# Kernel optimization log

Measured on AMD Instinct MI355X. Metric: run time of the kernel, lower is better.

The kernel has to match this reference:

```python
import jax, jax.numpy as jnp
import numpy as np

VOCAB, EMBED, HIDDEN = 32000, 256, 512
B, T = 8, 512


def setup_inputs() -> dict:
    key = jax.random.key(0)
    ks = jax.random.split(key, 7)
    x = jax.random.randint(ks[0], (B, T), 0, VOCAB)
    emb = jax.random.normal(ks[1], (VOCAB, EMBED), dtype=jnp.float32)
    W_xh = jax.random.normal(ks[2], (EMBED, HIDDEN), dtype=jnp.float32) * 0.01
    W_hh = jax.random.normal(ks[3], (HIDDEN, HIDDEN), dtype=jnp.float32) * 0.01
    b_h = jnp.zeros((HIDDEN,), dtype=jnp.float32)
    # nn.Linear(hidden*2, vocab): weight [vocab, 2*hidden], bias [vocab]
    lim = 1.0 / np.sqrt(2 * HIDDEN)
    fc_w = jax.random.uniform(ks[4], (VOCAB, 2 * HIDDEN), minval=-lim, maxval=lim, dtype=jnp.float32)
    fc_b = jax.random.uniform(ks[5], (VOCAB,), minval=-lim, maxval=lim, dtype=jnp.float32)
    return {"x": x, "emb": emb, "W_xh": W_xh, "W_hh": W_hh, "b_h": b_h, "fc_w": fc_w, "fc_b": fc_b}


def reference(x, emb, W_xh, W_hh, b_h, fc_w, fc_b):
    e = emb[x]  # [B,T,E]
    h0 = jnp.zeros((x.shape[0], W_hh.shape[0]), dtype=e.dtype)

    def step(h, xt):  # xt: [B,E]
        h = jnp.tanh(xt @ W_xh + h @ W_hh + b_h)
        return h, h

    _, H = jax.lax.scan(step, h0, jnp.swapaxes(e, 0, 1))  # H: [T,B,Hd]
    H = jnp.swapaxes(H, 0, 1)  # [B,T,Hd]
    # full (non-causal) dot-product self-attention over hidden states
    scores = jnp.einsum('bth,bsh->bts', H, H)  # [B,T,T]
    attn = jax.nn.softmax(scores, axis=-1)
    ctx = jnp.einsum('bts,bsh->bth', attn, H)  # [B,T,Hd]
    combined = jnp.concatenate([H, ctx], axis=-1)  # [B,T,2Hd]
    return combined @ fc_w.T + fc_b  # [B,T,V]
```

## Files before the change

### kernel.cpp

```cpp
#include <hip/hip_runtime.h>

typedef unsigned int u32;
typedef unsigned short u16;
typedef short bf16x8 __attribute__((ext_vector_type(8)));
typedef float f32x4 __attribute__((ext_vector_type(4)));

#define DEV __device__ __forceinline__

DEV u16 f2bf(float f) {
  u32 u = __builtin_bit_cast(u32, f);
  u += 0x7fffu + ((u >> 16) & 1u);
  return (u16)(u >> 16);
}
DEV float bf2f(u16 b) { u32 u = ((u32)b) << 16; return __builtin_bit_cast(float, u); }

DEV float dot2bf(float acc, u32 w, u32 h) {
  asm("v_dot2_f32_bf16 %0, %1, %2, %0" : "+v"(acc) : "v"(w), "v"(h));
  return acc;
}

DEV void gload16(const void* g, void* l) {
  __builtin_amdgcn_global_load_lds(
      (__attribute__((address_space(1))) void*)(void*)g,
      (__attribute__((address_space(3))) void*)l, 16, 0, 0);
}

__global__ void k_prep_fcw(const float* __restrict__ w, u16* __restrict__ o, int n4) {
  int i = blockIdx.x * blockDim.x + threadIdx.x;
  int stride = gridDim.x * blockDim.x;
  for (; i < n4; i += stride) {
    float4 v = ((const float4*)w)[i];
    ushort4 r; r.x = f2bf(v.x); r.y = f2bf(v.y); r.z = f2bf(v.z); r.w = f2bf(v.w);
    ((ushort4*)o)[i] = r;
  }
}

#define PREG 184
#define PLQ  18

__global__ void k_prep_whh(const float* __restrict__ w, u32* __restrict__ wr, u32* __restrict__ wq) {
  int idx = blockIdx.x * 256 + threadIdx.x;
  int p = idx >> 9, j = idx & 511;
  u32 word = (u32)f2bf(w[(2 * p) * 512 + j]) | ((u32)f2bf(w[(2 * p + 1) * 512 + j]) << 16);
  if (p < PREG) wr[p * 512 + j] = word;
  else { int d = p - PREG; wq[((d >> 2) * 512 + j) * 4 + (d & 3)] = word; }
}

__global__ __launch_bounds__(256) void k_embx(
    const int* __restrict__ x, const float* __restrict__ emb,
    const float* __restrict__ wxh, const float* __restrict__ bh,
    float* __restrict__ X) {
  __shared__ float sA[64][65];
  __shared__ __align__(16) float sB[64][68];
  int tid = threadIdx.x;
  int row0 = blockIdx.x * 64, col0 = blockIdx.y * 64;
  int tx = tid & 15, ty = tid >> 4;
  f32x4 acc[4] = {};
  for (int kc = 0; kc < 256; kc += 64) {
    __syncthreads();
#pragma unroll
    for (int i = 0; i < 4; ++i) {
      int f = i * 256 + tid;
      int r = f >> 4, c4 = (f & 15) * 4;
      int xr = x[row0 + r];
      float4 v = *(const float4*)&emb[(size_t)xr * 256 + kc + c4];
      sA[r][c4 + 0] = v.x; sA[r][c4 + 1] = v.y; sA[r][c4 + 2] = v.z; sA[r][c4 + 3] = v.w;
      float4 u = *(const float4*)&wxh[(size_t)(kc + r) * 512 + col0 + c4];
      *(float4*)&sB[r][c4] = u;
    }
    __syncthreads();
#pragma unroll
    for (int e = 0; e < 64; ++e) {
      f32x4 bv = *(const f32x4*)&sB[e][tx * 4];
      float a0 = sA[ty * 4 + 0][e], a1 = sA[ty * 4 + 1][e];
      float a2 = sA[ty * 4 + 2][e], a3 = sA[ty * 4 + 3][e];
      acc[0] += a0 * bv; acc[1] += a1 * bv; acc[2] += a2 * bv; acc[3] += a3 * bv;
    }
  }
  f32x4 bh4 = *(const f32x4*)&bh[col0 + tx * 4];
#pragma unroll
  for (int a = 0; a < 4; ++a) {
    f32x4 r = acc[a] + bh4;
    *(f32x4*)&X[(size_t)(row0 + ty * 4 + a) * 512 + col0 + tx * 4] = r;
  }
}

__global__ __launch_bounds__(512)
__attribute__((amdgpu_waves_per_eu(2, 2)))
void k_rnn(
    const u32* __restrict__ Wr, const u32* __restrict__ Wq,
    const float* __restrict__ X,
    u16* __restrict__ Hb16 ) {
  __shared__ __align__(16) u32 wl[PLQ * 512 * 4];
  __shared__ __align__(16) u32 hHI[2][256];
  __shared__ __align__(16) u32 hLO[2][256];
  int j = threadIdx.x;
  int b = blockIdx.x;
  u32 wreg[PREG];
#pragma unroll
  for (int p = 0; p < PREG; ++p) wreg[p] = Wr[p * 512 + j];
#pragma unroll
  for (int q = 0; q < PLQ; ++q)
    *(uint4*)&wl[(q * 512 + j) * 4] = *(const uint4*)&Wq[(q * 512 + j) * 4];
  if (j < 256) { hHI[0][j] = 0u; hLO[0][j] = 0u; }
  const float* Xb = X + (size_t)b * 512 * 512;
  u16* Hb = Hb16 + (size_t)b * 512 * 1024;
  __syncthreads();
  int cur = 0;
  float xv = Xb[j];
  for (int t = 0; t < 512; ++t) {
    int tn = t < 511 ? t + 1 : 511;
    float xnext = Xb[tn * 512 + j];
    float a0 = 0.f, a1 = 0.f, a2 = 0.f, a3 = 0.f;
    const u32* hbH = hHI[cur];
    const u32* hbL = hLO[cur];
#pragma unroll
    for (int c = 0; c < PREG / 4; ++c) {
      uint4 hH = *(const uint4*)&hbH[c * 4];
      uint4 hL = *(const uint4*)&hbL[c * 4];
      a0 = dot2bf(dot2bf(a0, wreg[c * 4 + 0], hH.x), wreg[c * 4 + 0], hL.x);
      a1 = dot2bf(dot2bf(a1, wreg[c * 4 + 1], hH.y), wreg[c * 4 + 1], hL.y);
      a2 = dot2bf(dot2bf(a2, wreg[c * 4 + 2], hH.z), wreg[c * 4 + 2], hL.z);
      a3 = dot2bf(dot2bf(a3, wreg[c * 4 + 3], hH.w), wreg[c * 4 + 3], hL.w);
    }
#pragma unroll
    for (int q = 0; q < PLQ; ++q) {
      uint4 wv = *(const uint4*)&wl[(q * 512 + j) * 4];
      uint4 hH = *(const uint4*)&hbH[PREG + q * 4];
      uint4 hL = *(const uint4*)&hbL[PREG + q * 4];
      a0 = dot2bf(dot2bf(a0, wv.x, hH.x), wv.x, hL.x);
      a1 = dot2bf(dot2bf(a1, wv.y, hH.y), wv.y, hL.y);
      a2 = dot2bf(dot2bf(a2, wv.z, hH.z), wv.z, hL.z);
      a3 = dot2bf(dot2bf(a3, wv.w, hH.w), wv.w, hL.w);
    }
    float z = xv + ((a0 + a1) + (a2 + a3));
    float ez = __expf(2.f * z);
    float h = 1.f - 2.f / (ez + 1.f);
    u16 hi = f2bf(h);
    u16 lo = f2bf(h - bf2f(hi));
    Hb[t * 1024 + j] = hi;
    ((u16*)hHI[cur ^ 1])[j] = hi;
    ((u16*)hLO[cur ^ 1])[j] = lo;
    __syncthreads();
    cur ^= 1;
    xv = xnext;
  }
}

template <int BF16OUT, int BIAS, int BF32B>
__global__ __launch_bounds__(256) void k_gemm_bt(
    const u16* __restrict__ A, int lda, long long aStr,
    const void* __restrict__ Bt_, int ldb, long long bStr,
    void* __restrict__ Cv, int ldc, long long cStr,
    int numMt, int numNt, int K, const float* __restrict__ bias) {
  __shared__ __align__(16) u16 lA[128 * 64];
  __shared__ __align__(16) u16 lB[128 * 64];
  int tid = threadIdx.x;
  int lane = tid & 63, wid = tid >> 6;
  int nwg = gridDim.x, wg = blockIdx.x;
  int q = nwg >> 3;
  int swz = (wg & 7) * q + (wg >> 3);
  int gm = numMt < 8 ? numMt : 8;
  int perg = gm * numNt;
  int grp = swz / perg;
  int rem = swz - grp * perg;
  int mt = grp * gm + rem % gm;
  int nt = rem / gm;
  int mrow = mt * 128, ncol = nt * 128;
  long long batch = blockIdx.y;
  A += batch * aStr;
  const u16* Bh = (const u16*)Bt_ + (BF32B ? 0 : batch * bStr);
  const float* Bf = (const float*)Bt_ + (BF32B ? batch * bStr : 0);
  float* Cf = (float*)Cv + batch * cStr;
  u16* Ch = (u16*)Cv + batch * cStr;

  f32x4 acc[4][4] = {};
  int wr = wid >> 1, wc = wid & 1;
  int lr = lane & 15, lk = (lane >> 4) * 8;

  for (int kt = 0; kt < K; kt += 64) {
    __syncthreads();
#pragma unroll
    for (int i = 0; i < 4; ++i) {
      int chunk = wid * 4 + i;
      int idx = chunk * 64 + lane;
      int r = idx >> 3, c = (idx & 7) * 8;
      gload16(&A[(size_t)(mrow + r) * lda + kt + c], &lA[chunk * 512]);
    }
    if constexpr (!BF32B) {
#pragma unroll
      for (int i = 0; i < 4; ++i) {
        int chunk = wid * 4 + i;
        int idx = chunk * 64 + lane;
        int r = idx >> 3, c = (idx & 7) * 8;
        gload16(&Bh[(size_t)(ncol + r) * ldb + kt + c], &lB[chunk * 512]);
      }
    } else {
#pragma unroll
      for (int u = 0; u < 8; ++u) {
        int flat = u * 1024 + tid * 4;
        int r = flat >> 6, c = flat & 63;
        float4 v = *(const float4*)&Bf[(size_t)(ncol + r) * ldb + kt + c];
        uint2 pk;
        pk.x = (u32)f2bf(v.x) | ((u32)f2bf(v.y) << 16);
        pk.y = (u32)f2bf(v.z) | ((u32)f2bf(v.w) << 16);
        *(uint2*)&lB[r * 64 + c] = pk;
      }
    }
    __syncthreads();
#pragma unroll
    for (int ks = 0; ks < 2; ++ks) {
      bf16x8 aF[4], bF[4];
#pragma unroll
      for (int mi = 0; mi < 4; ++mi)
        aF[mi] = *(const bf16x8*)&lA[(wr * 64 + mi * 16 + lr) * 64 + ks * 32 + lk];
#pragma unroll
      for (int ni = 0; ni < 4; ++ni)
        bF[ni] = *(const bf16x8*)&lB[(wc * 64 + ni * 16 + lr) * 64 + ks * 32 + lk];
#pragma unroll
      for (int mi = 0; mi < 4; ++mi)
#pragma unroll
        for (int ni = 0; ni < 4; ++ni)
          acc[mi][ni] = __builtin_amdgcn_mfma_f32_16x16x32_bf16(aF[mi], bF[ni], acc[mi][ni], 0, 0, 0);
    }
  }
  int rq = (lane >> 4) * 4;
#pragma unroll
  for (int ni = 0; ni < 4; ++ni) {
    int col = ncol + wc * 64 + ni * 16 + lr;
    float bv = BIAS ? bias[col] : 0.f;
#pragma unroll
    for (int mi = 0; mi < 4; ++mi) {
      int row = mrow + wr * 64 + mi * 16 + rq;
#pragma unroll
      for (int qq = 0; qq < 4; ++qq) {
        float v = acc[mi][ni][qq] + bv;
        if (BF16OUT) Ch[(size_t)(row + qq) * ldc + col] = f2bf(v);
        else         Cf[(size_t)(row + qq) * ldc + col] = v;
      }
    }
  }
}

DEV void stage_half(const u16* __restrict__ G, int ldg, int grow0, int kcol0,
                    u16* region, int w, int lane) {
#pragma unroll
  for (int jj = 0; jj < 2; ++jj) {
    int fb = jj * 512 + w * 64;
    int f = fb + lane;
    int r = f >> 2, s = f & 3;
    int c = (s ^ ((r >> 1) & 3)) * 8;
    gload16(&G[(size_t)(grow0 + r) * ldg + kcol0 + c], region + (size_t)fb * 8);
  }
}
DEV bf16x8 lds_frag(const u16* region, int r, int lq) {
  return *(const bf16x8*)&region[r * 32 + ((lq ^ ((r >> 1) & 3)) * 8)];
}

__global__ __launch_bounds__(512, 2) void k_gemm8(
    const u16* __restrict__ A, int lda,
    const u16* __restrict__ B, int ldb,
    float* __restrict__ C, int ldc,
    int numMt, int numNt, int K, const float* __restrict__ bias) {
  __shared__ __align__(16) u16 lds8[65536];
  int tid = threadIdx.x;
  int lane = tid & 63, wid = tid >> 6;
  int w = wid, wm = wid >> 2, wn = wid & 3;
  int lr = lane & 15, lq = lane >> 4;
  int nwg = gridDim.x, wg = blockIdx.x;
  int qd = nwg >> 3;
  int swz = (wg & 7) * qd + (wg >> 3);
  int gm = numMt < 8 ? numMt : 8;
  int perg = gm * numNt;
  int grp = swz / perg;
  int rem = swz - grp * perg;
  int mt = grp * gm + rem % gm;
  int nt = rem / gm;
  int mrow = mt * 256, ncol = nt * 256;
  int NT = K >> 6;

#define REGION(buf, op, kh) (lds8 + (((buf) * 2 + (op)) * 2 + (kh)) * 8192)

  f32x4 acc[8][4];
#pragma unroll
  for (int mi = 0; mi < 8; ++mi)
#pragma unroll
    for (int ni = 0; ni < 4; ++ni) acc[mi][ni] = (f32x4){0.f, 0.f, 0.f, 0.f};

  stage_half(A, lda, mrow, 0,  REGION(0, 0, 0), w, lane);
  stage_half(B, ldb, ncol, 0,  REGION(0, 1, 0), w, lane);
  stage_half(A, lda, mrow, 32, REGION(0, 0, 1), w, lane);
  stage_half(B, ldb, ncol, 32, REGION(0, 1, 1), w, lane);
  stage_half(A, lda, mrow, 64, REGION(1, 0, 0), w, lane);
  stage_half(B, ldb, ncol, 64, REGION(1, 1, 0), w, lane);
  asm volatile("s_waitcnt vmcnt(4)" ::: "memory");
  __builtin_amdgcn_s_barrier();
  asm volatile("" ::: "memory");

  for (int T = 0; T < NT; ++T) {
    int buf = T & 1;
    int s12 = (T + 1 < NT), s34 = (T + 2 < NT);
#pragma unroll
    for (int ph = 0; ph < 4; ++ph) {
      int ch = ph & 1, ks = ph >> 1;
      const u16* Ar = REGION(buf, 0, ks);
      const u16* Br = REGION(buf, 1, ks);
      bf16x8 aF[8], bF[2];
#pragma unroll
      for (int mi = 0; mi < 8; ++mi)
        aF[mi] = lds_frag(Ar, wm * 128 + mi * 16 + lr, lq);
#pragma unroll
      for (int nl = 0; nl < 2; ++nl)
        bF[nl] = lds_frag(Br, wn * 64 + (ch * 2 + nl) * 16 + lr, lq);
      if (ph == 0) { if (s12) stage_half(A, lda, mrow, (T + 1) * 64 + 32, REGION(buf ^ 1, 0, 1), w, lane); }
      if (ph == 1) { if (s12) stage_half(B, ldb, ncol, (T + 1) * 64 + 32, REGION(buf ^ 1, 1, 1), w, lane); }
      if (ph == 2) { if (s34) stage_half(A, lda, mrow, (T + 2) * 64,      REGION(buf, 0, 0),     w, lane); }
      if (ph == 3) { if (s34) stage_half(B, ldb, ncol, (T + 2) * 64,      REGION(buf, 1, 0),     w, lane); }
      asm volatile("" ::: "memory");
      __builtin_amdgcn_s_barrier();
      asm volatile("s_waitcnt lgkmcnt(0)" ::: "memory");
      __builtin_amdgcn_sched_barrier(0);
      __builtin_amdgcn_s_setprio(1);
#pragma unroll
      for (int mi = 0; mi < 8; ++mi) {
        acc[mi][ch * 2 + 0] = __builtin_amdgcn_mfma_f32_16x16x32_bf16(aF[mi], bF[0], acc[mi][ch * 2 + 0], 0, 0, 0);
        acc[mi][ch * 2 + 1] = __builtin_amdgcn_mfma_f32_16x16x32_bf16(aF[mi], bF[1], acc[mi][ch * 2 + 1], 0, 0, 0);
      }
      __builtin_amdgcn_s_setprio(0);
      if (ph == 3) {
        if (T >= NT - 2) asm volatile("s_waitcnt vmcnt(0)" ::: "memory");
        else             asm volatile("s_waitcnt vmcnt(4)" ::: "memory");
      }
      asm volatile("" ::: "memory");
      __builtin_amdgcn_s_barrier();
      asm volatile("" ::: "memory");
    }
  }
#undef REGION

#pragma unroll
  for (int mi = 0; mi < 8; ++mi) {
    int row0 = mrow + wm * 128 + mi * 16 + lq * 4;
#pragma unroll
    for (int ni = 0; ni < 4; ++ni) {
      int col = ncol + wn * 64 + ni * 16 + lr;
      float bv = bias[col];
#pragma unroll
      for (int rg = 0; rg < 4; ++rg)
        C[(size_t)(row0 + rg) * ldc + col] = acc[mi][ni][rg] + bv;
    }
  }
}

__global__ __launch_bounds__(256) void k_softmax(const float* __restrict__ S, u16* __restrict__ P) {
  int wid = threadIdx.x >> 6, lane = threadIdx.x & 63;
  int row = blockIdx.x * 4 + wid;
  const float* sr = S + (size_t)row * 512;
  f32x4 v0 = *(const f32x4*)&sr[lane * 4];
  f32x4 v1 = *(const f32x4*)&sr[256 + lane * 4];
  float m = fmaxf(fmaxf(fmaxf(v0.x, v0.y), fmaxf(v0.z, v0.w)),
                  fmaxf(fmaxf(v1.x, v1.y), fmaxf(v1.z, v1.w)));
#pragma unroll
  for (int o = 32; o; o >>= 1) m = fmaxf(m, __shfl_xor(m, o, 64));
  f32x4 e0, e1;
  e0.x = __expf(v0.x - m); e0.y = __expf(v0.y - m); e0.z = __expf(v0.z - m); e0.w = __expf(v0.w - m);
  e1.x = __expf(v1.x - m); e1.y = __expf(v1.y - m); e1.z = __expf(v1.z - m); e1.w = __expf(v1.w - m);
  float s = (e0.x + e0.y + e0.z + e0.w) + (e1.x + e1.y + e1.z + e1.w);
#pragma unroll
  for (int o = 32; o; o >>= 1) s += __shfl_xor(s, o, 64);
  float inv = 1.f / s;
  ushort4 o0, o1;
  o0.x = f2bf(e0.x * inv); o0.y = f2bf(e0.y * inv); o0.z = f2bf(e0.z * inv); o0.w = f2bf(e0.w * inv);
  o1.x = f2bf(e1.x * inv); o1.y = f2bf(e1.y * inv); o1.z = f2bf(e1.z * inv); o1.w = f2bf(e1.w * inv);
  *(ushort4*)&P[(size_t)row * 512 + lane * 4] = o0;
  *(ushort4*)&P[(size_t)row * 512 + 256 + lane * 4] = o1;
}

__global__ __launch_bounds__(256) void k_transpose(const u16* __restrict__ Hsrc, u16* __restrict__ HT) {
  __shared__ __align__(16) u16 tile[64][72];
  int b = blockIdx.z;
  int sb = blockIdx.x * 64, hb = blockIdx.y * 64;
  int tid = threadIdx.x;
#pragma unroll
  for (int i = 0; i < 4; ++i) {
    int f = i * 256 + tid; int r = f >> 4, c4 = (f & 15) * 4;
    ushort4 v = *(const ushort4*)&Hsrc[((size_t)(b * 512 + sb + r)) * 1024 + hb + c4];
    *(ushort4*)&tile[r][c4] = v;
  }
  __syncthreads();
#pragma unroll
  for (int i = 0; i < 4; ++i) {
    int f = i * 256 + tid; int h = f >> 4, s4 = (f & 15) * 4;
    ushort4 v;
    v.x = tile[s4 + 0][h]; v.y = tile[s4 + 1][h]; v.z = tile[s4 + 2][h]; v.w = tile[s4 + 3][h];
    *(ushort4*)&HT[((size_t)(b * 512 + hb + h)) * 512 + sb + s4] = v;
  }
}

extern "C" void kernel_launch(void* const* d_in, const int* in_sizes, int n_in,
                              void* d_out, int out_size, void* d_ws, size_t ws_size,
                              hipStream_t stream) {
  const int*   x   = (const int*)d_in[0];
  const float* emb = (const float*)d_in[1];
  const float* wxh = (const float*)d_in[2];
  const float* whh = (const float*)d_in[3];
  const float* bh  = (const float*)d_in[4];
  const float* fcw = (const float*)d_in[5];
  const float* fcb = (const float*)d_in[6];
  float* out = (float*)d_out;

  char* ws = (char*)d_ws;
  u32* Wr  = (u32*)ws;
  u32* Wq  = (u32*)(ws + 376832);
  u16* comb = (u16*)(ws + 524288);
  u16* fcwb = (u16*)(ws + 524288 + 8388608);
  bool bigws = ws_size >= (size_t)(524288 + 8388608 + 65536000);
  char* ob = (char*)d_out;
  float* X  = (float*)ob;
  float* S  = (float*)(ob + 8388608);
  u16*   P  = (u16*)(ob + 16777216);
  u16*   HT = (u16*)(ob + 20971520);

  k_prep_whh<<<dim3(512), dim3(256), 0, stream>>>(whh, Wr, Wq);
  k_embx<<<dim3(64, 8), dim3(256), 0, stream>>>(x, emb, wxh, bh, X);
  if (bigws)
    k_prep_fcw<<<dim3(2048), dim3(256), 0, stream>>>(fcw, fcwb, 8192000);
  k_rnn<<<dim3(8), dim3(512), 0, stream>>>(Wr, Wq, X, comb);
  k_gemm_bt<0, 0, 0><<<dim3(16, 8), dim3(256), 0, stream>>>(
      comb, 1024, 512LL * 1024, comb, 1024, 512LL * 1024,
      (void*)S, 512, 512LL * 512, 4, 4, 512, (const float*)nullptr);
  k_softmax<<<dim3(1024), dim3(256), 0, stream>>>(S, P);
  k_transpose<<<dim3(8, 8, 8), dim3(256), 0, stream>>>(comb, HT);
  k_gemm_bt<1, 0, 0><<<dim3(16, 8), dim3(256), 0, stream>>>(
      P, 512, 512LL * 512, HT, 512, 512LL * 512,
      (void*)(comb + 512), 1024, 512LL * 1024, 4, 4, 512, (const float*)nullptr);
  if (bigws)
    k_gemm8<<<dim3(2000), dim3(512), 0, stream>>>(
        comb, 1024, fcwb, 1024, out, 32000, 16, 125, 1024, fcb);
  else
    k_gemm_bt<0, 1, 1><<<dim3(8000), dim3(256), 0, stream>>>(
        comb, 1024, 0LL, fcw, 1024, 0LL,
        (void*)out, 32000, 0LL, 32, 250, 1024, fcb);
}
```

Baseline: 1.648 ms.

## Broadcast recurrent hidden state via readlane into SGPR operands for RNN dot products

The recurrent step now has each lane load just two uint4 chunks of an interleaved hi/lo hidden-state buffer, instead of every thread reading the whole hidden vector from LDS with uniform-address loads. Each h value is then broadcast to the wave with v_readlane and passed to v_dot2 as a scalar operand. This layout interleaves the hi and lo bf16 words so one pair of vector loads per lane covers the full 512-element state. It trades LDS traffic for many readlane instructions on the serial critical path, and hardcodes 46 register chunks, which must match PREG.

Result: slower. 2.695 ms (+63.5%).

```diff
diff --git a/kernel.cpp b/kernel.cpp
--- a/kernel.cpp
+++ b/kernel.cpp
@@ -14,8 +14,8 @@
 }
 DEV float bf2f(u16 b) { u32 u = ((u32)b) << 16; return __builtin_bit_cast(float, u); }
 
-DEV float dot2bf(float acc, u32 w, u32 h) {
-  asm("v_dot2_f32_bf16 %0, %1, %2, %0" : "+v"(acc) : "v"(w), "v"(h));
+DEV float dot2bf_s(float acc, u32 w, u32 h_uni) {
+  asm("v_dot2_f32_bf16 %0, %1, %2, %0" : "+v"(acc) : "s"(h_uni), "v"(w));
   return acc;
 }
 
@@ -92,9 +92,8 @@
     const float* __restrict__ X,
     u16* __restrict__ Hb16 ) {
   __shared__ __align__(16) u32 wl[PLQ * 512 * 4];
-  __shared__ __align__(16) u32 hHI[2][256];
-  __shared__ __align__(16) u32 hLO[2][256];
-  int j = threadIdx.x;
+  __shared__ __align__(16) u32 hch[2][512];
+  int j = threadIdx.x, lane = j & 63;
   int b = blockIdx.x;
   u32 wreg[PREG];
 #pragma unroll
@@ -102,7 +101,8 @@
 #pragma unroll
   for (int q = 0; q < PLQ; ++q)
     *(uint4*)&wl[(q * 512 + j) * 4] = *(const uint4*)&Wq[(q * 512 + j) * 4];
-  if (j < 256) { hHI[0][j] = 0u; hLO[0][j] = 0u; }
+  hch[0][j] = 0u;
+  int wc16 = (j >> 3) * 16 + ((j >> 1) & 3) * 2 + (j & 1);
   const float* Xb = X + (size_t)b * 512 * 512;
   u16* Hb = Hb16 + (size_t)b * 512 * 1024;
   __syncthreads();
@@ -111,27 +111,40 @@
   for (int t = 0; t < 512; ++t) {
     int tn = t < 511 ? t + 1 : 511;
     float xnext = Xb[tn * 512 + j];
+    uint4 chA = *(const uint4*)&hch[cur][lane * 8];
+    uint4 chB = *(const uint4*)&hch[cur][lane * 8 + 4];
     float a0 = 0.f, a1 = 0.f, a2 = 0.f, a3 = 0.f;
-    const u32* hbH = hHI[cur];
-    const u32* hbL = hLO[cur];
-#pragma unroll
-    for (int c = 0; c < PREG / 4; ++c) {
-      uint4 hH = *(const uint4*)&hbH[c * 4];
-      uint4 hL = *(const uint4*)&hbL[c * 4];
-      a0 = dot2bf(dot2bf(a0, wreg[c * 4 + 0], hH.x), wreg[c * 4 + 0], hL.x);
-      a1 = dot2bf(dot2bf(a1, wreg[c * 4 + 1], hH.y), wreg[c * 4 + 1], hL.y);
-      a2 = dot2bf(dot2bf(a2, wreg[c * 4 + 2], hH.z), wreg[c * 4 + 2], hL.z);
-      a3 = dot2bf(dot2bf(a3, wreg[c * 4 + 3], hH.w), wreg[c * 4 + 3], hL.w);
-    }
-#pragma unroll
-    for (int q = 0; q < PLQ; ++q) {
+#pragma unroll
+    for (int c = 0; c < 46; ++c) {
+      u32 h0 = (u32)__builtin_amdgcn_readlane((int)chA.x, c);
+      u32 h1 = (u32)__builtin_amdgcn_readlane((int)chA.y, c);
+      u32 h2 = (u32)__builtin_amdgcn_readlane((int)chA.z, c);
+      u32 h3 = (u32)__builtin_amdgcn_readlane((int)chA.w, c);
+      u32 l0 = (u32)__builtin_amdgcn_readlane((int)chB.x, c);
+      u32 l1 = (u32)__builtin_amdgcn_readlane((int)chB.y, c);
+      u32 l2 = (u32)__builtin_amdgcn_readlane((int)chB.z, c);
+      u32 l3 = (u32)__builtin_amdgcn_readlane((int)chB.w, c);
+      a0 = dot2bf_s(dot2bf_s(a0, wreg[c * 4 + 0], h0), wreg[c * 4 + 0], l0);
+      a1 = dot2bf_s(dot2bf_s(a1, wreg[c * 4 + 1], h1), wreg[c * 4 + 1], l1);
+      a2 = dot2bf_s(dot2bf_s(a2, wreg[c * 4 + 2], h2), wreg[c * 4 + 2], l2);
+      a3 = dot2bf_s(dot2bf_s(a3, wreg[c * 4 + 3], h3), wreg[c * 4 + 3], l3);
+    }
+#pragma unroll
+    for (int c = 46; c < 64; ++c) {
+      int q = c - 46;
       uint4 wv = *(const uint4*)&wl[(q * 512 + j) * 4];
-      uint4 hH = *(const uint4*)&hbH[PREG + q * 4];
-      uint4 hL = *(const uint4*)&hbL[PREG + q * 4];
-      a0 = dot2bf(dot2bf(a0, wv.x, hH.x), wv.x, hL.x);
-      a1 = dot2bf(dot2bf(a1, wv.y, hH.y), wv.y, hL.y);
-      a2 = dot2bf(dot2bf(a2, wv.z, hH.z), wv.z, hL.z);
-      a3 = dot2bf(dot2bf(a3, wv.w, hH.w), wv.w, hL.w);
+      u32 h0 = (u32)__builtin_amdgcn_readlane((int)chA.x, c);
+      u32 h1 = (u32)__builtin_amdgcn_readlane((int)chA.y, c);
+      u32 h2 = (u32)__builtin_amdgcn_readlane((int)chA.z, c);
+      u32 h3 = (u32)__builtin_amdgcn_readlane((int)chA.w, c);
+      u32 l0 = (u32)__builtin_amdgcn_readlane((int)chB.x, c);
+      u32 l1 = (u32)__builtin_amdgcn_readlane((int)chB.y, c);
+      u32 l2 = (u32)__builtin_amdgcn_readlane((int)chB.z, c);
+      u32 l3 = (u32)__builtin_amdgcn_readlane((int)chB.w, c);
+      a0 = dot2bf_s(dot2bf_s(a0, wv.x, h0), wv.x, l0);
+      a1 = dot2bf_s(dot2bf_s(a1, wv.y, h1), wv.y, l1);
+      a2 = dot2bf_s(dot2bf_s(a2, wv.z, h2), wv.z, l2);
+      a3 = dot2bf_s(dot2bf_s(a3, wv.w, h3), wv.w, l3);
     }
     float z = xv + ((a0 + a1) + (a2 + a3));
     float ez = __expf(2.f * z);
@@ -139,8 +152,9 @@
     u16 hi = f2bf(h);
     u16 lo = f2bf(h - bf2f(hi));
     Hb[t * 1024 + j] = hi;
-    ((u16*)hHI[cur ^ 1])[j] = hi;
-    ((u16*)hLO[cur ^ 1])[j] = lo;
+    u16* hw = (u16*)&hch[cur ^ 1][0];
+    hw[wc16] = hi;
+    hw[wc16 + 8] = lo;
     __syncthreads();
     cur ^= 1;
     xv = xnext;
```

## Hold all W_hh in registers and overlap fc_w conversion with RNN kernel

Applied to the files above, without the earlier changes.

Two changes. The fc_w fp32→bf16 conversion moves into extra blocks of the RNN kernel, so it runs on idle CUs while the 8 latency-bound recurrence blocks execute, and its separate launch and serialized time go away. The recurrent weights are now held entirely in registers (256 words per thread), which drops the LDS-resident part and its per-step LDS weight reads. The risks are register spilling, given 256 weight registers plus the rest under a 2-waves-per-EU cap, and the conversion blocks competing for memory bandwidth or CU placement with the RNN blocks.

After: 3.269 ms. +98.3%, slower.

```diff
diff --git a/kernel.cpp b/kernel.cpp
--- a/kernel.cpp
+++ b/kernel.cpp
@@ -25,25 +25,13 @@
       (__attribute__((address_space(3))) void*)l, 16, 0, 0);
 }
 
-__global__ void k_prep_fcw(const float* __restrict__ w, u16* __restrict__ o, int n4) {
-  int i = blockIdx.x * blockDim.x + threadIdx.x;
-  int stride = gridDim.x * blockDim.x;
-  for (; i < n4; i += stride) {
-    float4 v = ((const float4*)w)[i];
-    ushort4 r; r.x = f2bf(v.x); r.y = f2bf(v.y); r.z = f2bf(v.z); r.w = f2bf(v.w);
-    ((ushort4*)o)[i] = r;
-  }
-}
-
-#define PREG 184
-#define PLQ  18
-
-__global__ void k_prep_whh(const float* __restrict__ w, u32* __restrict__ wr, u32* __restrict__ wq) {
+#define PREG 256
+
+__global__ void k_prep_whh(const float* __restrict__ w, u32* __restrict__ wr) {
   int idx = blockIdx.x * 256 + threadIdx.x;
   int p = idx >> 9, j = idx & 511;
   u32 word = (u32)f2bf(w[(2 * p) * 512 + j]) | ((u32)f2bf(w[(2 * p + 1) * 512 + j]) << 16);
-  if (p < PREG) wr[p * 512 + j] = word;
-  else { int d = p - PREG; wq[((d >> 2) * 512 + j) * 4 + (d & 3)] = word; }
+  wr[p * 512 + j] = word;
 }
 
 __global__ __launch_bounds__(256) void k_embx(
@@ -88,10 +76,21 @@
 __global__ __launch_bounds__(512)
 __attribute__((amdgpu_waves_per_eu(2, 2)))
 void k_rnn(
-    const u32* __restrict__ Wr, const u32* __restrict__ Wq,
-    const float* __restrict__ X,
-    u16* __restrict__ Hb16 ) {
-  __shared__ __align__(16) u32 wl[PLQ * 512 * 4];
+    const u32* __restrict__ Wr, const float* __restrict__ X,
+    u16* __restrict__ Hb16 ,
+    const float* __restrict__ fcw, u16* __restrict__ fcwb) {
+  if (blockIdx.x >= 8) {
+    if (fcwb) {
+      int i = (blockIdx.x - 8) * 512 + threadIdx.x;
+      int stride = (gridDim.x - 8) * 512;
+      for (; i < 8192000; i += stride) {
+        float4 v = ((const float4*)fcw)[i];
+        ushort4 r; r.x = f2bf(v.x); r.y = f2bf(v.y); r.z = f2bf(v.z); r.w = f2bf(v.w);
+        ((ushort4*)fcwb)[i] = r;
+      }
+    }
+    return;
+  }
   __shared__ __align__(16) u32 hHI[2][256];
   __shared__ __align__(16) u32 hLO[2][256];
   int j = threadIdx.x;
@@ -99,9 +98,6 @@
   u32 wreg[PREG];
 #pragma unroll
   for (int p = 0; p < PREG; ++p) wreg[p] = Wr[p * 512 + j];
-#pragma unroll
-  for (int q = 0; q < PLQ; ++q)
-    *(uint4*)&wl[(q * 512 + j) * 4] = *(const uint4*)&Wq[(q * 512 + j) * 4];
   if (j < 256) { hHI[0][j] = 0u; hLO[0][j] = 0u; }
   const float* Xb = X + (size_t)b * 512 * 512;
   u16* Hb = Hb16 + (size_t)b * 512 * 1024;
@@ -115,23 +111,13 @@
     const u32* hbH = hHI[cur];
     const u32* hbL = hLO[cur];
 #pragma unroll
-    for (int c = 0; c < PREG / 4; ++c) {
+    for (int c = 0; c < 64; ++c) {
       uint4 hH = *(const uint4*)&hbH[c * 4];
       uint4 hL = *(const uint4*)&hbL[c * 4];
       a0 = dot2bf(dot2bf(a0, wreg[c * 4 + 0], hH.x), wreg[c * 4 + 0], hL.x);
       a1 = dot2bf(dot2bf(a1, wreg[c * 4 + 1], hH.y), wreg[c * 4 + 1], hL.y);
       a2 = dot2bf(dot2bf(a2, wreg[c * 4 + 2], hH.z), wreg[c * 4 + 2], hL.z);
       a3 = dot2bf(dot2bf(a3, wreg[c * 4 + 3], hH.w), wreg[c * 4 + 3], hL.w);
-    }
-#pragma unroll
-    for (int q = 0; q < PLQ; ++q) {
-      uint4 wv = *(const uint4*)&wl[(q * 512 + j) * 4];
-      uint4 hH = *(const uint4*)&hbH[PREG + q * 4];
-      uint4 hL = *(const uint4*)&hbL[PREG + q * 4];
-      a0 = dot2bf(dot2bf(a0, wv.x, hH.x), wv.x, hL.x);
-      a1 = dot2bf(dot2bf(a1, wv.y, hH.y), wv.y, hL.y);
-      a2 = dot2bf(dot2bf(a2, wv.z, hH.z), wv.z, hL.z);
-      a3 = dot2bf(dot2bf(a3, wv.w, hH.w), wv.w, hL.w);
     }
     float z = xv + ((a0 + a1) + (a2 + a3));
     float ez = __expf(2.f * z);
@@ -411,7 +397,6 @@
 
   char* ws = (char*)d_ws;
   u32* Wr  = (u32*)ws;
-  u32* Wq  = (u32*)(ws + 376832);
   u16* comb = (u16*)(ws + 524288);
   u16* fcwb = (u16*)(ws + 524288 + 8388608);
   bool bigws = ws_size >= (size_t)(524288 + 8388608 + 65536000);
@@ -421,11 +406,10 @@
   u16*   P  = (u16*)(ob + 16777216);
   u16*   HT = (u16*)(ob + 20971520);
 
-  k_prep_whh<<<dim3(512), dim3(256), 0, stream>>>(whh, Wr, Wq);
+  k_prep_whh<<<dim3(512), dim3(256), 0, stream>>>(whh, Wr);
   k_embx<<<dim3(64, 8), dim3(256), 0, stream>>>(x, emb, wxh, bh, X);
-  if (bigws)
-    k_prep_fcw<<<dim3(2048), dim3(256), 0, stream>>>(fcw, fcwb, 8192000);
-  k_rnn<<<dim3(8), dim3(512), 0, stream>>>(Wr, Wq, X, comb);
+  k_rnn<<<dim3(bigws ? 1024 : 8), dim3(512), 0, stream>>>(
+      Wr, X, comb, fcw, bigws ? fcwb : (u16*)nullptr);
   k_gemm_bt<0, 0, 0><<<dim3(16, 8), dim3(256), 0, stream>>>(
       comb, 1024, 512LL * 1024, comb, 1024, 512LL * 1024,
       (void*)S, 512, 512LL * 512, 4, 4, 512, (const float*)nullptr);
```
